# Performance work log

Hardware: AMD Instinct MI355X
Metric: run time of the kernel (lower is better)

## Reference

```python
import jax, jax.numpy as jnp
import numpy as np

B = 16777216

def setup_inputs() -> dict:
    key = jax.random.key(0)
    k1, k2 = jax.random.split(key)
    x = jax.random.normal(k1, (B, 2), dtype=jnp.float32)
    ws = jax.random.normal(k2, (10,), dtype=jnp.float32)  # 10 scalar Linear(1,1) weights
    return {"x": x, "ws": ws}

def _step(carry, w):
    x0, x1 = carry
    nx0 = x0 - 0.1 * x1
    nx1 = 0.1 * x0 + x1 - 0.1 * x0**3 + 0.1 * (w * x1)
    return (nx0, nx1), None

def reference(x, ws):
    (x0, x1), _ = jax.lax.scan(_step, (x[:, 0], x[:, 1]), ws)
    out = (jnp.tanh(100.0 * (x1 - 0.1)) - jnp.tanh(100.0 * (x1 + 0.1)) + 2.0) / 2.0
    return out[:, None]  # [B, 1]
```

## Files before the change

kernel.cpp:

```cpp
#include <hip/hip_runtime.h>

__device__ __forceinline__ float band(float x1) {
    float E  = __builtin_amdgcn_exp2f(fmaf(288.539008f, x1, 28.8539008f));
    float Eu = E * 4.248354255291589e-18f;
    return 1.0f + __builtin_amdgcn_rcpf(E + 1.0f) - __builtin_amdgcn_rcpf(Eu + 1.0f);
}

__device__ __forceinline__ void traj(float& a0, float& a1, const float* __restrict__ w01) {
#pragma unroll
    for (int k = 0; k < 10; ++k) {
        float na0 = fmaf(-0.1f, a1, a0);
        float s   = a0 * a0;
        float c   = s * a0;
        float t1  = fmaf(0.1f, a0, a1);
        float t2  = fmaf(-0.1f, c, t1);
        float na1 = fmaf(w01[k], a1, t2);
        a0 = na0; a1 = na1;
    }
}

__global__ void __launch_bounds__(256)
dynsys_kernel(const float4* __restrict__ x, const float* __restrict__ ws,
              float2* __restrict__ out, int half) {
    int i = blockIdx.x * 256 + threadIdx.x;
    if (i >= half) return;

    float w01[10];
#pragma unroll
    for (int k = 0; k < 10; ++k) w01[k] = 0.1f * ws[k];

    float4 va = x[i];
    float4 vb = x[i + half];

    float a0 = va.x, a1 = va.y; traj(a0, a1, w01);
    float b0 = va.z, b1 = va.w; traj(b0, b1, w01);
    float c0 = vb.x, c1 = vb.y; traj(c0, c1, w01);
    float d0 = vb.z, d1 = vb.w; traj(d0, d1, w01);

    out[i]        = make_float2(band(a1), band(b1));
    out[i + half] = make_float2(band(c1), band(d1));
}

extern "C" void kernel_launch(void* const* d_in, const int* in_sizes, int n_in,
                              void* d_out, int out_size, void* d_ws, size_t ws_size,
                              hipStream_t stream) {
    const float4* x  = (const float4*)d_in[0];
    const float*  ws = (const float*)d_in[1];
    float2* out = (float2*)d_out;

    int n4   = in_sizes[0] / 4;
    int half = n4 / 2;
    int blocks = (half + 255) / 256;
    dynsys_kernel<<<blocks, 256, 0, stream>>>(x, ws, out, half);
}
```

Before: 208.2 us.

## Vectorize trajectory math with packed float2 ops and process 8 rows per thread

Rewrites the 10-step recurrence on two-wide vector types so the compiler can emit packed FP32 instructions (v_pk_fma_f32 / v_pk_mul_f32) that handle two trajectories per instruction. Each thread now loads four float4s (8 rows) from four quarter-strided regions instead of two, which halves the grid size. The aim is to cut ALU instruction count and raise memory-level parallelism per thread. The cost is more live registers per thread and fewer threads overall.

Measured after the change: 212.5 us. 1.02x slower.

```diff
diff --git a/kernel.cpp b/kernel.cpp
--- a/kernel.cpp
+++ b/kernel.cpp
@@ -1,4 +1,11 @@
 #include <hip/hip_runtime.h>
+
+typedef float v2 __attribute__((ext_vector_type(2)));
+
+__device__ __forceinline__ v2 splat(float s) { v2 r; r.x = s; r.y = s; return r; }
+__device__ __forceinline__ v2 vfma(v2 a, v2 b, v2 c) {
+    return __builtin_elementwise_fma(a, b, c);
+}
 
 __device__ __forceinline__ float band(float x1) {
     float E  = __builtin_amdgcn_exp2f(fmaf(288.539008f, x1, 28.8539008f));
@@ -6,39 +13,48 @@
     return 1.0f + __builtin_amdgcn_rcpf(E + 1.0f) - __builtin_amdgcn_rcpf(Eu + 1.0f);
 }
 
-__device__ __forceinline__ void traj(float& a0, float& a1, const float* __restrict__ w01) {
+__device__ __forceinline__ void traj2(v2& a0, v2& a1, const v2* __restrict__ w01) {
 #pragma unroll
     for (int k = 0; k < 10; ++k) {
-        float na0 = fmaf(-0.1f, a1, a0);
-        float s   = a0 * a0;
-        float c   = s * a0;
-        float t1  = fmaf(0.1f, a0, a1);
-        float t2  = fmaf(-0.1f, c, t1);
-        float na1 = fmaf(w01[k], a1, t2);
+        v2 na0 = vfma(splat(-0.1f), a1, a0);
+        v2 s   = a0 * a0;
+        v2 c   = s * a0;
+        v2 t1  = vfma(splat(0.1f), a0, a1);
+        v2 t2  = vfma(splat(-0.1f), c, t1);
+        v2 na1 = vfma(w01[k], a1, t2);
         a0 = na0; a1 = na1;
     }
 }
 
 __global__ void __launch_bounds__(256)
 dynsys_kernel(const float4* __restrict__ x, const float* __restrict__ ws,
-              float2* __restrict__ out, int half) {
+              float2* __restrict__ out, int q) {
     int i = blockIdx.x * 256 + threadIdx.x;
-    if (i >= half) return;
+    if (i >= q) return;
 
-    float w01[10];
+    v2 w01[10];
 #pragma unroll
-    for (int k = 0; k < 10; ++k) w01[k] = 0.1f * ws[k];
+    for (int k = 0; k < 10; ++k) w01[k] = splat(0.1f * ws[k]);
 
     float4 va = x[i];
-    float4 vb = x[i + half];
+    float4 vb = x[i + q];
+    float4 vc = x[i + 2 * q];
+    float4 vd = x[i + 3 * q];
 
-    float a0 = va.x, a1 = va.y; traj(a0, a1, w01);
-    float b0 = va.z, b1 = va.w; traj(b0, b1, w01);
-    float c0 = vb.x, c1 = vb.y; traj(c0, c1, w01);
-    float d0 = vb.z, d1 = vb.w; traj(d0, d1, w01);
+    v2 a0 = {va.x, va.z}, a1 = {va.y, va.w};
+    v2 b0 = {vb.x, vb.z}, b1 = {vb.y, vb.w};
+    v2 c0 = {vc.x, vc.z}, c1 = {vc.y, vc.w};
+    v2 d0 = {vd.x, vd.z}, d1 = {vd.y, vd.w};
 
-    out[i]        = make_float2(band(a1), band(b1));
-    out[i + half] = make_float2(band(c1), band(d1));
+    traj2(a0, a1, w01);
+    traj2(b0, b1, w01);
+    traj2(c0, c1, w01);
+    traj2(d0, d1, w01);
+
+    out[i]         = make_float2(band(a1.x), band(a1.y));
+    out[i + q]     = make_float2(band(b1.x), band(b1.y));
+    out[i + 2 * q] = make_float2(band(c1.x), band(c1.y));
+    out[i + 3 * q] = make_float2(band(d1.x), band(d1.y));
 }
 
 extern "C" void kernel_launch(void* const* d_in, const int* in_sizes, int n_in,
@@ -48,8 +64,8 @@
     const float*  ws = (const float*)d_in[1];
     float2* out = (float2*)d_out;
 
-    int n4   = in_sizes[0] / 4;
-    int half = n4 / 2;
-    int blocks = (half + 255) / 256;
-    dynsys_kernel<<<blocks, 256, 0, stream>>>(x, ws, out, half);
+    int n4 = in_sizes[0] / 4;
+    int q  = n4 / 4;
+    int blocks = (q + 255) / 256;
+    dynsys_kernel<<<blocks, 256, 0, stream>>>(x, ws, out, q);
 }
```

## Use packed f32 FMA math and process eight float4 per thread

Applied to the files above, without the earlier changes.

Rewrites the 10-step recurrence with v_pk_fma_f32/v_pk_mul_f32 inline asm, so two trajectories advance per instruction. The per-step algebra is regrouped to five packed ops: x1 + 0.1*(x0 - x0^3 + w*x1) with the sign folded into negated weights. Each thread now loads eight float4 values up front and writes its results with nontemporal stores. This aims to halve the VALU instruction count and deepen memory-level parallelism, at the cost of more registers per thread, fewer threads, and slight rounding differences from the reassociation.

Measured after the change: 214.0 us. 1.03x slower.

```diff
diff --git a/kernel.cpp b/kernel.cpp
--- a/kernel.cpp
+++ b/kernel.cpp
@@ -1,4 +1,17 @@
 #include <hip/hip_runtime.h>
+
+typedef float v2f __attribute__((ext_vector_type(2)));
+
+__device__ __forceinline__ v2f pk_fma(v2f a, v2f b, v2f c) {
+    v2f d;
+    asm("v_pk_fma_f32 %0, %1, %2, %3" : "=v"(d) : "v"(a), "v"(b), "v"(c));
+    return d;
+}
+__device__ __forceinline__ v2f pk_mul(v2f a, v2f b) {
+    v2f d;
+    asm("v_pk_mul_f32 %0, %1, %2" : "=v"(d) : "v"(a), "v"(b));
+    return d;
+}
 
 __device__ __forceinline__ float band(float x1) {
     float E  = __builtin_amdgcn_exp2f(fmaf(288.539008f, x1, 28.8539008f));
@@ -6,39 +19,38 @@
     return 1.0f + __builtin_amdgcn_rcpf(E + 1.0f) - __builtin_amdgcn_rcpf(Eu + 1.0f);
 }
 
-__device__ __forceinline__ void traj(float& a0, float& a1, const float* __restrict__ w01) {
-#pragma unroll
-    for (int k = 0; k < 10; ++k) {
-        float na0 = fmaf(-0.1f, a1, a0);
-        float s   = a0 * a0;
-        float c   = s * a0;
-        float t1  = fmaf(0.1f, a0, a1);
-        float t2  = fmaf(-0.1f, c, t1);
-        float na1 = fmaf(w01[k], a1, t2);
-        a0 = na0; a1 = na1;
-    }
-}
-
 __global__ void __launch_bounds__(256)
 dynsys_kernel(const float4* __restrict__ x, const float* __restrict__ ws,
-              float2* __restrict__ out, int half) {
+              v2f* __restrict__ out, int T) {
     int i = blockIdx.x * 256 + threadIdx.x;
-    if (i >= half) return;
+    if (i >= T) return;
 
-    float w01[10];
+    v2f wn[10];
 #pragma unroll
-    for (int k = 0; k < 10; ++k) w01[k] = 0.1f * ws[k];
+    for (int k = 0; k < 10; ++k) { float v = -ws[k]; wn[k] = (v2f){v, v}; }
+    const v2f mone = {-1.0f, -1.0f};
+    const v2f cn01 = {-0.1f, -0.1f};
 
-    float4 va = x[i];
-    float4 vb = x[i + half];
+    float4 ld[8];
+#pragma unroll
+    for (int k = 0; k < 8; ++k) ld[k] = x[i + k * T];
 
-    float a0 = va.x, a1 = va.y; traj(a0, a1, w01);
-    float b0 = va.z, b1 = va.w; traj(b0, b1, w01);
-    float c0 = vb.x, c1 = vb.y; traj(c0, c1, w01);
-    float d0 = vb.z, d1 = vb.w; traj(d0, d1, w01);
-
-    out[i]        = make_float2(band(a1), band(b1));
-    out[i + half] = make_float2(band(c1), band(d1));
+#pragma unroll
+    for (int k = 0; k < 8; ++k) {
+        v2f a0 = {ld[k].x, ld[k].z};
+        v2f a1 = {ld[k].y, ld[k].w};
+#pragma unroll
+        for (int s = 0; s < 10; ++s) {
+            v2f na0 = pk_fma(cn01, a1, a0);
+            v2f t   = pk_fma(a0, a0, mone);
+            v2f u   = pk_mul(a0, t);
+            v2f d   = pk_fma(wn[s], a1, u);
+            a1      = pk_fma(cn01, d, a1);
+            a0      = na0;
+        }
+        v2f r = {band(a1.x), band(a1.y)};
+        __builtin_nontemporal_store(r, &out[i + k * T]);
+    }
 }
 
 extern "C" void kernel_launch(void* const* d_in, const int* in_sizes, int n_in,
@@ -46,10 +58,10 @@
                               hipStream_t stream) {
     const float4* x  = (const float4*)d_in[0];
     const float*  ws = (const float*)d_in[1];
-    float2* out = (float2*)d_out;
+    v2f* out = (v2f*)d_out;
 
-    int n4   = in_sizes[0] / 4;
-    int half = n4 / 2;
-    int blocks = (half + 255) / 256;
-    dynsys_kernel<<<blocks, 256, 0, stream>>>(x, ws, out, half);
+    int n4 = in_sizes[0] / 4;
+    int T  = n4 / 8;
+    int blocks = (T + 255) / 256;
+    dynsys_kernel<<<blocks, 256, 0, stream>>>(x, ws, out, T);
 }
```
